# Kernel optimization log

Measured on AMD Instinct MI355X. Metric: run time of the kernel, lower is better.

## Reference

```python
import jax, jax.numpy as jnp
import numpy as np

D = 192          # d_model
H = 8            # n_heads
DH = D // H      # d_head = 24
DFF = 2 * D      # FeedForward hidden = d_model*2
SIZES = [384 + 8 * i for i in range(32)]   # ragged segment lengths
TOTAL = sum(SIZES)                          # 16256
EPS = 1e-5

# static ragged -> padded index maps (numpy, baked at trace time)
_sz = np.asarray(SIZES)
B = len(_sz)
MAXN = int(_sz.max())
SEG = np.repeat(np.arange(B), _sz)                      # [TOTAL] segment id
POS = np.concatenate([np.arange(s) for s in _sz])       # [TOTAL] position in segment
PADMASK = np.ones((B, MAXN), dtype=bool)                # True = padding (key_padding_mask)
PADMASK[SEG, POS] = False


def _layernorm(x, gamma, beta):
    mu = jnp.mean(x, axis=-1, keepdims=True)
    var = jnp.var(x, axis=-1, keepdims=True)
    return (x - mu) * jax.lax.rsqrt(var + EPS) * gamma + beta


def setup_inputs() -> dict:
    key = jax.random.key(0)
    ks = jax.random.split(key, 8)
    w = lambda k, shape: jax.random.normal(k, shape, jnp.float32) * 0.02
    return {
        "x": jax.random.normal(ks[0], (TOTAL, D), jnp.float32),
        "sizes": jnp.asarray(SIZES, jnp.int32),
        "Wqkv": w(ks[1], (3 * D, D)), "bqkv": jnp.zeros((3 * D,), jnp.float32),
        "Wo": w(ks[2], (D, D)),       "bo": jnp.zeros((D,), jnp.float32),
        "Wg": w(ks[3], (D, 2 * D)),   "bg": jnp.zeros((D,), jnp.float32),
        "gamma1": jnp.ones((D,), jnp.float32), "beta1": jnp.zeros((D,), jnp.float32),
        "W1": w(ks[4], (DFF, D)),     "b1": jnp.zeros((DFF,), jnp.float32),
        "W2": w(ks[5], (D, DFF)),     "b2": jnp.zeros((D,), jnp.float32),
        "gamma2": jnp.ones((D,), jnp.float32), "beta2": jnp.zeros((D,), jnp.float32),
    }


def reference(x, sizes, Wqkv, bqkv, Wo, bo, Wg, bg, gamma1, beta1,
              W1, b1, W2, b2, gamma2, beta2):
    # --- pad_by_sizes (vectorized scatter, static index maps) ---
    pad = jnp.zeros((B, MAXN, D), x.dtype).at[SEG, POS].set(x)   # [B, MAXN, D]

    # --- nn.MultiheadAttention (batch_first, key_padding_mask) ---
    qkv = pad @ Wqkv.T + bqkv                                    # [B, MAXN, 3D]
    q, k, v = jnp.split(qkv, 3, axis=-1)
    def heads(t):  # [B, MAXN, D] -> [B, H, MAXN, DH]
        return t.reshape(B, MAXN, H, DH).transpose(0, 2, 1, 3)
    q, k, v = heads(q), heads(k), heads(v)
    scores = jnp.einsum("bhqd,bhkd->bhqk", q, k) / np.sqrt(DH)   # [B, H, MAXN, MAXN]
    scores = jnp.where(PADMASK[:, None, None, :], jnp.float32(-1e9), scores)
    attn = jax.nn.softmax(scores, axis=-1)
    o = jnp.einsum("bhqk,bhkd->bhqd", attn, v)                   # [B, H, MAXN, DH]
    o = o.transpose(0, 2, 1, 3).reshape(B, MAXN, D)
    out = o @ Wo.T + bo                                          # [B, MAXN, D]

    # --- gather back to ragged; gate/norm/ff are per-token, so the torch
    # per-segment loop is equivalent to one vectorized pass over all tokens ---
    out_flat = out[SEG, POS]                                     # [TOTAL, D]
    g = jax.nn.sigmoid(jnp.concatenate([out_flat, x], axis=-1) @ Wg.T + bg)
    h = g * out_flat + (1.0 - g) * x                             # GatedResidual
    h = _layernorm(h, gamma1, beta1)                             # self.norm
    y = jax.nn.silu(h @ W1.T + b1) @ W2.T + b2                   # FeedForward.net
    return _layernorm(h + y, gamma2, beta2)                      # residual + norm
```

## Files before the change

kernel.cpp:

```cpp
#include <hip/hip_runtime.h>
#include <hip/hip_bf16.h>
#include <math.h>

#define D_      192
#define H_      8
#define DH_     24
#define NSEG    32
#define TOTAL_  16256
static constexpr float LN_EPS = 1e-5f;
static constexpr float SCALE  = 0.20412414523193154f;
static constexpr float SC_L2E = 0.29446679331797463f;

typedef float  f32x4  __attribute__((ext_vector_type(4)));
typedef short  bf16x8 __attribute__((ext_vector_type(8)));
typedef unsigned short u16x4 __attribute__((ext_vector_type(4)));
typedef unsigned int   u32x4 __attribute__((ext_vector_type(4)));

__device__ __forceinline__ unsigned short f2b(float f) {
    __hip_bfloat16 h = __float2bfloat16(f);
    return *(unsigned short*)&h;
}
__device__ __forceinline__ unsigned pack2(float a, float b) {
    __hip_bfloat162 h = __float22bfloat162_rn(make_float2(a, b));
    return *(unsigned*)&h;
}
__device__ __forceinline__ float b2f(unsigned short h) {
    union { unsigned u; float f; } v; v.u = (unsigned)h << 16; return v.f;
}
__device__ __forceinline__ float fexp2(float x) {
#if __has_builtin(__builtin_amdgcn_exp2f)
    return __builtin_amdgcn_exp2f(x);
#else
    return exp2f(x);
#endif
}

#define NXE 3121152
__global__ __launch_bounds__(256)
void conv_all(const float* __restrict__ x,
              const float* __restrict__ w0, const float* __restrict__ w1,
              const float* __restrict__ w2, const float* __restrict__ w3,
              const float* __restrict__ w4,
              unsigned short* __restrict__ xb, unsigned short* __restrict__ wb)
{
    int i = (blockIdx.x * 256 + threadIdx.x) * 4;
    const float* src; unsigned short* dst; int off;
    if (i < NXE) { src = x; dst = xb; off = 0; }
    else {
        int j = i - NXE; dst = wb;
        if      (j < 110592) { src = w0; off = 0; }
        else if (j < 147456) { src = w1; off = 110592; }
        else if (j < 221184) { src = w2; off = 147456; }
        else if (j < 294912) { src = w3; off = 221184; }
        else                 { src = w4; off = 294912; }
        i = j;
    }
    float4 v = *(const float4*)&src[i - off];
    u16x4 o = { f2b(v.x), f2b(v.y), f2b(v.z), f2b(v.w) };
    *(u16x4*)&dst[i] = o;
}

template<int KF, int MR, int OUT_BF16>
__global__ __launch_bounds__(256)
void gemm_lds(const unsigned short* __restrict__ Ain,
              const unsigned short* __restrict__ Wb,
              const float* __restrict__ bias,
              void* __restrict__ Cout, int N)
{
    constexpr int KSW = KF * 32 + 8;
    __shared__ unsigned short Wp[64 * KSW];

    const int tid = threadIdx.x;
    const int wv  = tid >> 6;
    const int l   = tid & 63;
    const int m0  = blockIdx.x * (64 * MR) + wv * (16 * MR);
    const int n0  = blockIdx.y * 64;
    const int rl  = l & 15;
    const int kc  = (l >> 4) * 8;

    bf16x8 afrag[MR][KF];
    #pragma unroll
    for (int h = 0; h < MR; ++h)
        #pragma unroll
        for (int kk = 0; kk < KF; ++kk)
            afrag[h][kk] = *(const bf16x8*)&Ain[(size_t)(m0 + h * 16 + rl) * (KF * 32) + kk * 32 + kc];

    #pragma unroll
    for (int i = 0; i < KF; ++i) {
        int u = i * 256 + tid;
        int row = u / (KF * 4), c = u % (KF * 4);
        *(bf16x8*)&Wp[row * KSW + c * 8] = *(const bf16x8*)&Wb[(size_t)(n0 + row) * (KF * 32) + c * 8];
    }
    __syncthreads();

    f32x4 acc[MR][4] = {};
    #pragma unroll
    for (int kk = 0; kk < KF; ++kk) {
        #pragma unroll
        for (int nf = 0; nf < 4; ++nf) {
            bf16x8 b = *(const bf16x8*)&Wp[(nf * 16 + rl) * KSW + kk * 32 + kc];
            #pragma unroll
            for (int h = 0; h < MR; ++h)
                acc[h][nf] = __builtin_amdgcn_mfma_f32_16x16x32_bf16(afrag[h][kk], b, acc[h][nf], 0, 0, 0);
        }
    }

    #pragma unroll
    for (int h = 0; h < MR; ++h) {
        #pragma unroll
        for (int nf = 0; nf < 4; ++nf) {
            const int c = n0 + nf * 16 + rl;
            const float bz = bias[c];
            #pragma unroll
            for (int q = 0; q < 4; ++q) {
                const int r = m0 + h * 16 + (l >> 4) * 4 + q;
                float v = acc[h][nf][q] + bz;
                if (OUT_BF16) ((unsigned short*)Cout)[(size_t)r * N + c] = f2b(v);
                else          ((float*)Cout)[(size_t)r * N + c] = v;
            }
        }
    }
}

__global__ __launch_bounds__(256, 2)
void tail_fused(const unsigned short* __restrict__ o_b,
                const unsigned short* __restrict__ xb,
                const unsigned short* __restrict__ wo_b,
                const unsigned short* __restrict__ wg_b,
                const unsigned short* __restrict__ w1_b,
                const unsigned short* __restrict__ w2_b,
                const float* __restrict__ bo, const float* __restrict__ bg,
                const float* __restrict__ b1, const float* __restrict__ b2,
                const float* __restrict__ gamma1, const float* __restrict__ beta1,
                const float* __restrict__ gamma2, const float* __restrict__ beta2,
                float* __restrict__ out)
{
    constexpr int WS = 200;
    __shared__ unsigned short Wp[96 * WS];
    __shared__ unsigned short Al[64 * WS];

    const int tid = threadIdx.x;
    const int wv  = tid >> 6;
    const int l   = tid & 63;
    const int rl  = l & 15;
    const int g   = l >> 4;
    const int kc  = g * 8;
    const int m0  = blockIdx.x * 64 + wv * 16;

    bf16x8 afA[6];
    #pragma unroll
    for (int kk = 0; kk < 6; ++kk)
        afA[kk] = *(const bf16x8*)&o_b[(size_t)(m0 + rl) * 192 + kk * 32 + kc];

    f32x4 accA[12] = {};
    #pragma unroll
    for (int sub = 0; sub < 2; ++sub) {
        __syncthreads();
        #pragma unroll
        for (int i = 0; i < 9; ++i) {
            int u = i * 256 + tid;
            int row = u / 24, c = u % 24;
            *(bf16x8*)&Wp[row * WS + c * 8] = *(const bf16x8*)&wo_b[(size_t)(sub * 96 + row) * 192 + c * 8];
        }
        __syncthreads();
        #pragma unroll
        for (int kk = 0; kk < 6; ++kk)
            #pragma unroll
            for (int nf2 = 0; nf2 < 6; ++nf2) {
                bf16x8 b = *(const bf16x8*)&Wp[(nf2 * 16 + rl) * WS + kk * 32 + kc];
                accA[sub * 6 + nf2] = __builtin_amdgcn_mfma_f32_16x16x32_bf16(afA[kk], b, accA[sub * 6 + nf2], 0, 0, 0);
            }
    }

    float att[12][4];
    #pragma unroll
    for (int nf = 0; nf < 12; ++nf) {
        const int cnf = (nf / 6) * 96 + (nf % 6) * 16 + rl;
        const float bz = bo[cnf];
        #pragma unroll
        for (int q = 0; q < 4; ++q) {
            att[nf][q] = accA[nf][q] + bz;
            Al[(wv * 16 + g * 4 + q) * WS + cnf] = f2b(att[nf][q]);
        }
    }

    bf16x8 afX[6];
    #pragma unroll
    for (int kk = 0; kk < 6; ++kk)
        afX[kk] = *(const bf16x8*)&xb[(size_t)(m0 + rl) * 192 + kk * 32 + kc];

    f32x4 accB[12] = {};
    #pragma unroll
    for (int kb2 = 0; kb2 < 2; ++kb2)
        #pragma unroll
        for (int sub = 0; sub < 2; ++sub) {
            __syncthreads();
            #pragma unroll
            for (int i = 0; i < 9; ++i) {
                int u = i * 256 + tid;
                int row = u / 24, c = u % 24;
                *(bf16x8*)&Wp[row * WS + c * 8] = *(const bf16x8*)&wg_b[(size_t)(sub * 96 + row) * 384 + kb2 * 192 + c * 8];
            }
            __syncthreads();
            #pragma unroll
            for (int kk = 0; kk < 6; ++kk) {
                bf16x8 a = (kb2 == 0) ? *(const bf16x8*)&Al[(wv * 16 + rl) * WS + kk * 32 + kc]
                                      : afX[kk];
                #pragma unroll
                for (int nf2 = 0; nf2 < 6; ++nf2) {
                    bf16x8 b = *(const bf16x8*)&Wp[(nf2 * 16 + rl) * WS + kk * 32 + kc];
                    accB[sub * 6 + nf2] = __builtin_amdgcn_mfma_f32_16x16x32_bf16(a, b, accB[sub * 6 + nf2], 0, 0, 0);
                }
            }
        }

    float h1ln[12][4];
    {
        float bz[12], gam[12], bet[12];
        #pragma unroll
        for (int nf = 0; nf < 12; ++nf) {
            const int cnf = (nf / 6) * 96 + (nf % 6) * 16 + rl;
            bz[nf]  = bg[cnf];
            gam[nf] = gamma1[cnf];
            bet[nf] = beta1[cnf];
        }
        #pragma unroll
        for (int q = 0; q < 4; ++q) {
            const int r = m0 + g * 4 + q;
            const size_t rb = (size_t)r * 192;
            float h[12];
            float s = 0.f;
            #pragma unroll
            for (int nf = 0; nf < 12; ++nf) {
                const int cnf = (nf / 6) * 96 + (nf % 6) * 16 + rl;
                float v  = accB[nf][q] + bz[nf];
                float gt = 1.f / (1.f + __expf(-v));
                h[nf] = gt * att[nf][q] + (1.f - gt) * b2f(xb[rb + cnf]);
                s += h[nf];
            }
            s += __shfl_xor(s, 1); s += __shfl_xor(s, 2);
            s += __shfl_xor(s, 4); s += __shfl_xor(s, 8);
            const float mu = s * (1.f / 192.f);
            float sq = 0.f;
            #pragma unroll
            for (int nf = 0; nf < 12; ++nf) { float d = h[nf] - mu; sq += d * d; }
            sq += __shfl_xor(sq, 1); sq += __shfl_xor(sq, 2);
            sq += __shfl_xor(sq, 4); sq += __shfl_xor(sq, 8);
            const float rstd = rsqrtf(sq * (1.f / 192.f) + LN_EPS);
            #pragma unroll
            for (int nf = 0; nf < 12; ++nf)
                h1ln[nf][q] = (h[nf] - mu) * rstd * gam[nf] + bet[nf];
        }
    }
    __syncthreads();
    #pragma unroll
    for (int nf = 0; nf < 12; ++nf) {
        const int cnf = (nf / 6) * 96 + (nf % 6) * 16 + rl;
        #pragma unroll
        for (int q = 0; q < 4; ++q)
            Al[(wv * 16 + g * 4 + q) * WS + cnf] = f2b(h1ln[nf][q]);
    }
    __syncthreads();

    bf16x8 afC[6];
    #pragma unroll
    for (int kk = 0; kk < 6; ++kk)
        afC[kk] = *(const bf16x8*)&Al[(wv * 16 + rl) * WS + kk * 32 + kc];

    f32x4 accD[12] = {};
    #pragma unroll
    for (int ch = 0; ch < 2; ++ch) {
        f32x4 accC[12] = {};
        #pragma unroll
        for (int sub = 0; sub < 2; ++sub) {
            __syncthreads();
            #pragma unroll
            for (int i = 0; i < 9; ++i) {
                int u = i * 256 + tid;
                int row = u / 24, c = u % 24;
                *(bf16x8*)&Wp[row * WS + c * 8] = *(const bf16x8*)&w1_b[(size_t)(ch * 192 + sub * 96 + row) * 192 + c * 8];
            }
            __syncthreads();
            #pragma unroll
            for (int kk = 0; kk < 6; ++kk)
                #pragma unroll
                for (int nf2 = 0; nf2 < 6; ++nf2) {
                    bf16x8 b = *(const bf16x8*)&Wp[(nf2 * 16 + rl) * WS + kk * 32 + kc];
                    accC[sub * 6 + nf2] = __builtin_amdgcn_mfma_f32_16x16x32_bf16(afC[kk], b, accC[sub * 6 + nf2], 0, 0, 0);
                }
        }
        __syncthreads();
        #pragma unroll
        for (int nf = 0; nf < 12; ++nf) {
            const int colc = (nf / 6) * 96 + (nf % 6) * 16 + rl;
            const float bz1 = b1[ch * 192 + colc];
            #pragma unroll
            for (int q = 0; q < 4; ++q) {
                float v = accC[nf][q] + bz1;
                float s = 1.f / (1.f + __expf(-v));
                Al[(wv * 16 + g * 4 + q) * WS + colc] = f2b(v * s);
            }
        }
        #pragma unroll
        for (int sub = 0; sub < 2; ++sub) {
            __syncthreads();
            #pragma unroll
            for (int i = 0; i < 9; ++i) {
                int u = i * 256 + tid;
                int row = u / 24, c = u % 24;
                *(bf16x8*)&Wp[row * WS + c * 8] = *(const bf16x8*)&w2_b[(size_t)(sub * 96 + row) * 384 + ch * 192 + c * 8];
            }
            __syncthreads();
            #pragma unroll
            for (int kk = 0; kk < 6; ++kk) {
                bf16x8 a = *(const bf16x8*)&Al[(wv * 16 + rl) * WS + kk * 32 + kc];
                #pragma unroll
                for (int nf2 = 0; nf2 < 6; ++nf2) {
                    bf16x8 b = *(const bf16x8*)&Wp[(nf2 * 16 + rl) * WS + kk * 32 + kc];
                    accD[sub * 6 + nf2] = __builtin_amdgcn_mfma_f32_16x16x32_bf16(a, b, accD[sub * 6 + nf2], 0, 0, 0);
                }
            }
        }
    }

    float bz[12], gam[12], bet[12];
    #pragma unroll
    for (int nf = 0; nf < 12; ++nf) {
        const int cnf = (nf / 6) * 96 + (nf % 6) * 16 + rl;
        bz[nf]  = b2[cnf];
        gam[nf] = gamma2[cnf];
        bet[nf] = beta2[cnf];
    }
    #pragma unroll
    for (int q = 0; q < 4; ++q) {
        const int r = m0 + g * 4 + q;
        const size_t rb = (size_t)r * 192;
        float h[12];
        float s = 0.f;
        #pragma unroll
        for (int nf = 0; nf < 12; ++nf) {
            h[nf] = h1ln[nf][q] + accD[nf][q] + bz[nf];
            s += h[nf];
        }
        s += __shfl_xor(s, 1); s += __shfl_xor(s, 2);
        s += __shfl_xor(s, 4); s += __shfl_xor(s, 8);
        const float mu = s * (1.f / 192.f);
        float sq = 0.f;
        #pragma unroll
        for (int nf = 0; nf < 12; ++nf) { float d = h[nf] - mu; sq += d * d; }
        sq += __shfl_xor(sq, 1); sq += __shfl_xor(sq, 2);
        sq += __shfl_xor(sq, 4); sq += __shfl_xor(sq, 8);
        const float rstd = rsqrtf(sq * (1.f / 192.f) + LN_EPS);
        #pragma unroll
        for (int nf = 0; nf < 12; ++nf) {
            const int cnf = (nf / 6) * 96 + (nf % 6) * 16 + rl;
            out[rb + cnf] = (h[nf] - mu) * rstd * gam[nf] + bet[nf];
        }
    }
}

#define KSTR 40
#define VSTR 72

__global__ __launch_bounds__(256)
void attn_mfma(const unsigned short* __restrict__ qkv, unsigned short* __restrict__ o)
{
    const int w    = blockIdx.x;
    const int xcd  = w & 7;
    const int slot = w >> 3;
    const int seg  = xcd + 8 * (slot / 80);
    const int inr  = slot % 80;
    const int head = inr / 10;
    const int q0   = (inr % 10) * 64;

    const int n    = 384 + 8 * seg;
    const int base = 384 * seg + 4 * seg * (seg - 1);
    if (q0 >= n) return;

    __shared__ unsigned short Ks[2][64 * KSTR];
    __shared__ unsigned short Vt[2][32 * VSTR];

    const int tid = threadIdx.x;
    const int wv  = tid >> 6;
    const int l   = tid & 63;
    const int lq  = l & 15;
    const int g   = l >> 4;

    if (tid < 64) {
        *(uint4*)&Ks[0][tid * KSTR + 24] = make_uint4(0, 0, 0, 0);
        *(uint4*)&Ks[1][tid * KSTR + 24] = make_uint4(0, 0, 0, 0);
    }
    for (int t4 = tid; t4 < 144; t4 += 256) {
        *(unsigned long long*)&Vt[0][24 * VSTR + t4 * 4] = 0ull;
        *(unsigned long long*)&Vt[1][24 * VSTR + t4 * 4] = 0ull;
    }

    const int qrow = q0 + wv * 16 + lq;
    const int qtok = base + (qrow < n ? qrow : n - 1);
    bf16x8 qfrag = {};
    if (g < 3) qfrag = *(const bf16x8*)&qkv[(size_t)qtok * 576 + head * 24 + g * 8];

    const int sj  = tid & 63;
    const int sc  = tid >> 6;
    const int scj = 32 * (sj >> 5) + 8 * ((sj >> 2) & 3) + 4 * ((sj >> 4) & 1) + (sj & 3);

    bf16x8 kreg = {}, vreg = {};
    if (tid < 192) {
        int jr = sj; if (jr >= n) jr = n - 1;
        const unsigned short* rp = &qkv[(size_t)(base + jr) * 576 + head * 24 + sc * 8];
        kreg = *(const bf16x8*)(rp + 192);
        vreg = *(const bf16x8*)(rp + 384);
        *(bf16x8*)&Ks[0][sj * KSTR + sc * 8] = kreg;
        #pragma unroll
        for (int e = 0; e < 8; ++e)
            Vt[0][(sc * 8 + e) * VSTR + scj] = ((const unsigned short*)&vreg)[e];
    }

    float lsum = 0.f;
    f32x4 oacc[2] = {};

    const int nt = (n + 63) >> 6;
    int cur = 0;
    for (int t = 0; t < nt; ++t) {
        __syncthreads();
        const int j0 = t * 64;
        const bool pf = (t + 1 < nt) && (tid < 192);
        if (pf) {
            int jr = j0 + 64 + sj; if (jr >= n) jr = n - 1;
            const unsigned short* rp = &qkv[(size_t)(base + jr) * 576 + head * 24 + sc * 8];
            kreg = *(const bf16x8*)(rp + 192);
            vreg = *(const bf16x8*)(rp + 384);
        }

        bf16x8 kf[4];
        #pragma unroll
        for (int ks = 0; ks < 4; ++ks)
            kf[ks] = *(const bf16x8*)&Ks[cur][(ks * 16 + lq) * KSTR + g * 8];

        const int rem = n - j0;
        f32x4 sacc[4] = {};
        #pragma unroll
        for (int ks = 0; ks < 4; ++ks)
            sacc[ks] = __builtin_amdgcn_mfma_f32_16x16x32_bf16(kf[ks], qfrag, sacc[ks], 0, 0, 0);

        float psum = 0.f;
        unsigned pw[8];
        #pragma unroll
        for (int ks = 0; ks < 4; ++ks) {
            float pv[4];
            #pragma unroll
            for (int r = 0; r < 4; ++r) {
                float p = fexp2(sacc[ks][r] * SC_L2E);
                if (rem < 64) { int key = ks * 16 + g * 4 + r; if (key >= rem) p = 0.f; }
                psum += p;
                pv[r] = p;
            }
            pw[ks * 2 + 0] = pack2(pv[0], pv[1]);
            pw[ks * 2 + 1] = pack2(pv[2], pv[3]);
        }
        psum += __shfl_xor(psum, 16);
        psum += __shfl_xor(psum, 32);
        lsum += psum;

        bf16x8 pfr[2];
        #pragma unroll
        for (int jk = 0; jk < 2; ++jk) {
            u32x4 fr = { pw[jk*4+0], pw[jk*4+1], pw[jk*4+2], pw[jk*4+3] };
            pfr[jk] = *(bf16x8*)&fr;
        }

        #pragma unroll
        for (int jk = 0; jk < 2; ++jk) {
            #pragma unroll
            for (int df = 0; df < 2; ++df) {
                bf16x8 vf = *(const bf16x8*)&Vt[cur][(df * 16 + lq) * VSTR + jk * 32 + g * 8];
                oacc[df] = __builtin_amdgcn_mfma_f32_16x16x32_bf16(vf, pfr[jk], oacc[df], 0, 0, 0);
            }
        }

        if (pf) {
            *(bf16x8*)&Ks[cur ^ 1][sj * KSTR + sc * 8] = kreg;
            #pragma unroll
            for (int e = 0; e < 8; ++e)
                Vt[cur ^ 1][(sc * 8 + e) * VSTR + scj] = ((const unsigned short*)&vreg)[e];
        }
        cur ^= 1;
    }

    if (qrow < n) {
        const float rl2 = 1.f / lsum;
        #pragma unroll
        for (int df = 0; df < 2; ++df) {
            const int d0 = df * 16 + g * 4;
            if (d0 < 24) {
                unsigned w0 = pack2(oacc[df][0] * rl2, oacc[df][1] * rl2);
                unsigned w1 = pack2(oacc[df][2] * rl2, oacc[df][3] * rl2);
                unsigned long long wd = (unsigned long long)w0 | ((unsigned long long)w1 << 32);
                *(unsigned long long*)&o[(size_t)(base + qrow) * 192 + head * 24 + d0] = wd;
            }
        }
    }
}

extern "C" void kernel_launch(void* const* d_in, const int* in_sizes, int n_in,
                              void* d_out, int out_size, void* d_ws, size_t ws_size,
                              hipStream_t stream)
{
    const float* x      = (const float*)d_in[0];
    const float* Wqkv   = (const float*)d_in[2];
    const float* bqkv   = (const float*)d_in[3];
    const float* Wo     = (const float*)d_in[4];
    const float* bo     = (const float*)d_in[5];
    const float* Wg     = (const float*)d_in[6];
    const float* bg     = (const float*)d_in[7];
    const float* gamma1 = (const float*)d_in[8];
    const float* beta1  = (const float*)d_in[9];
    const float* W1     = (const float*)d_in[10];
    const float* b1     = (const float*)d_in[11];
    const float* W2     = (const float*)d_in[12];
    const float* b2     = (const float*)d_in[13];
    const float* gamma2 = (const float*)d_in[14];
    const float* beta2  = (const float*)d_in[15];
    float* out = (float*)d_out;
    float* ws  = (float*)d_ws;

    const size_t T = TOTAL_;
    unsigned short* qkv_b = (unsigned short*)ws;
    unsigned short* o_b   = (unsigned short*)(ws + 288 * T);
    unsigned short* wb    = (unsigned short*)(ws + 384 * T);
    unsigned short* xb    = (unsigned short*)(ws + 396 * T);

    dim3 blk(256);

    conv_all<<<dim3(3408), blk, 0, stream>>>(x, Wqkv, Wo, Wg, W1, W2, xb, wb);
    gemm_lds<6,2,1><<<dim3(127, 9), blk, 0, stream>>>(xb, wb, bqkv, qkv_b, 576);
    attn_mfma<<<dim3(2560), blk, 0, stream>>>(qkv_b, o_b);
    tail_fused<<<dim3(254), blk, 0, stream>>>(o_b, xb, wb + 110592, wb + 147456,
                                              wb + 221184, wb + 294912,
                                              bo, bg, b1, b2,
                                              gamma1, beta1, gamma2, beta2, out);
}
```

Before: 91.94 us.

## Prefetch next weight tile into registers in tail kernel; fold softmax scale into QKV GEMM

The fused tail kernel is restructured into a flat sequence of weight-tile stages in which the next 96-row weight slab is loaded from global memory into registers while the current slab is consumed by MFMA sweeps. This hides global-load latency behind compute instead of serializing load, sync and compute, at the cost of nine extra bf16x8 registers per thread. Separately, the QKV GEMM now multiplies Q columns by scale*log2(e) in its epilogue, which removes a multiply per score in the attention inner loop. That change rounds the scaled Q to bf16, a small precision difference.

```diff
diff --git a/kernel.cpp b/kernel.cpp
--- a/kernel.cpp
+++ b/kernel.cpp
@@ -60,7 +60,7 @@
     *(u16x4*)&dst[i] = o;
 }
 
-template<int KF, int MR, int OUT_BF16>
+template<int KF, int MR, int OUT_BF16, int QS>
 __global__ __launch_bounds__(256)
 void gemm_lds(const unsigned short* __restrict__ Ain,
               const unsigned short* __restrict__ Wb,
@@ -115,12 +115,26 @@
             for (int q = 0; q < 4; ++q) {
                 const int r = m0 + h * 16 + (l >> 4) * 4 + q;
                 float v = acc[h][nf][q] + bz;
+                if (QS && c < 192) v *= SC_L2E;
                 if (OUT_BF16) ((unsigned short*)Cout)[(size_t)r * N + c] = f2b(v);
                 else          ((float*)Cout)[(size_t)r * N + c] = v;
             }
         }
     }
 }
+
+#define LOAD9(BASE, STRIDE) { \
+    _Pragma("unroll") for (int i_ = 0; i_ < 9; ++i_) \
+        wreg[i_] = *(const bf16x8*)&(BASE)[(size_t)rowA[i_] * (STRIDE) + colA[i_] * 8]; }
+#define STAGE9() { \
+    _Pragma("unroll") for (int i_ = 0; i_ < 9; ++i_) \
+        *(bf16x8*)&Wp[rowA[i_] * WS + colA[i_] * 8] = wreg[i_]; }
+#define SWEEP6(ACC, OFF, AEXPR) { \
+    _Pragma("unroll") for (int kk = 0; kk < 6; ++kk) { \
+        bf16x8 a_ = (AEXPR); \
+        _Pragma("unroll") for (int nf2 = 0; nf2 < 6; ++nf2) { \
+            bf16x8 b_ = *(const bf16x8*)&Wp[(nf2 * 16 + rl) * WS + kk * 32 + kc]; \
+            ACC[(OFF) + nf2] = __builtin_amdgcn_mfma_f32_16x16x32_bf16(a_, b_, ACC[(OFF) + nf2], 0, 0, 0); } } }
 
 __global__ __launch_bounds__(256, 2)
 void tail_fused(const unsigned short* __restrict__ o_b,
@@ -147,30 +161,25 @@
     const int kc  = g * 8;
     const int m0  = blockIdx.x * 64 + wv * 16;
 
-    bf16x8 afA[6];
-    #pragma unroll
-    for (int kk = 0; kk < 6; ++kk)
+    int rowA[9], colA[9];
+    #pragma unroll
+    for (int i = 0; i < 9; ++i) { int u = i * 256 + tid; rowA[i] = u / 24; colA[i] = u % 24; }
+    bf16x8 wreg[9];
+
+    bf16x8 afA[6], afX[6];
+    #pragma unroll
+    for (int kk = 0; kk < 6; ++kk) {
         afA[kk] = *(const bf16x8*)&o_b[(size_t)(m0 + rl) * 192 + kk * 32 + kc];
+        afX[kk] = *(const bf16x8*)&xb [(size_t)(m0 + rl) * 192 + kk * 32 + kc];
+    }
+
+    LOAD9(wo_b, 192);
 
     f32x4 accA[12] = {};
-    #pragma unroll
-    for (int sub = 0; sub < 2; ++sub) {
-        __syncthreads();
-        #pragma unroll
-        for (int i = 0; i < 9; ++i) {
-            int u = i * 256 + tid;
-            int row = u / 24, c = u % 24;
-            *(bf16x8*)&Wp[row * WS + c * 8] = *(const bf16x8*)&wo_b[(size_t)(sub * 96 + row) * 192 + c * 8];
-        }
-        __syncthreads();
-        #pragma unroll
-        for (int kk = 0; kk < 6; ++kk)
-            #pragma unroll
-            for (int nf2 = 0; nf2 < 6; ++nf2) {
-                bf16x8 b = *(const bf16x8*)&Wp[(nf2 * 16 + rl) * WS + kk * 32 + kc];
-                accA[sub * 6 + nf2] = __builtin_amdgcn_mfma_f32_16x16x32_bf16(afA[kk], b, accA[sub * 6 + nf2], 0, 0, 0);
-            }
-    }
+    STAGE9(); LOAD9(wo_b + 96 * 192, 192); __syncthreads();
+    SWEEP6(accA, 0, afA[kk]);
+    __syncthreads(); STAGE9(); LOAD9(wg_b, 384); __syncthreads();
+    SWEEP6(accA, 6, afA[kk]);
 
     float att[12][4];
     #pragma unroll
@@ -184,35 +193,15 @@
         }
     }
 
-    bf16x8 afX[6];
-    #pragma unroll
-    for (int kk = 0; kk < 6; ++kk)
-        afX[kk] = *(const bf16x8*)&xb[(size_t)(m0 + rl) * 192 + kk * 32 + kc];
-
     f32x4 accB[12] = {};
-    #pragma unroll
-    for (int kb2 = 0; kb2 < 2; ++kb2)
-        #pragma unroll
-        for (int sub = 0; sub < 2; ++sub) {
-            __syncthreads();
-            #pragma unroll
-            for (int i = 0; i < 9; ++i) {
-                int u = i * 256 + tid;
-                int row = u / 24, c = u % 24;
-                *(bf16x8*)&Wp[row * WS + c * 8] = *(const bf16x8*)&wg_b[(size_t)(sub * 96 + row) * 384 + kb2 * 192 + c * 8];
-            }
-            __syncthreads();
-            #pragma unroll
-            for (int kk = 0; kk < 6; ++kk) {
-                bf16x8 a = (kb2 == 0) ? *(const bf16x8*)&Al[(wv * 16 + rl) * WS + kk * 32 + kc]
-                                      : afX[kk];
-                #pragma unroll
-                for (int nf2 = 0; nf2 < 6; ++nf2) {
-                    bf16x8 b = *(const bf16x8*)&Wp[(nf2 * 16 + rl) * WS + kk * 32 + kc];
-                    accB[sub * 6 + nf2] = __builtin_amdgcn_mfma_f32_16x16x32_bf16(a, b, accB[sub * 6 + nf2], 0, 0, 0);
-                }
-            }
-        }
+    __syncthreads(); STAGE9(); LOAD9(wg_b + 96 * 384, 384); __syncthreads();
+    SWEEP6(accB, 0, (*(const bf16x8*)&Al[(wv * 16 + rl) * WS + kk * 32 + kc]));
+    __syncthreads(); STAGE9(); LOAD9(wg_b + 192, 384); __syncthreads();
+    SWEEP6(accB, 6, (*(const bf16x8*)&Al[(wv * 16 + rl) * WS + kk * 32 + kc]));
+    __syncthreads(); STAGE9(); LOAD9(wg_b + 96 * 384 + 192, 384); __syncthreads();
+    SWEEP6(accB, 0, afX[kk]);
+    __syncthreads(); STAGE9(); LOAD9(w1_b, 192); __syncthreads();
+    SWEEP6(accB, 6, afX[kk]);
 
     float h1ln[12][4];
     {
@@ -252,7 +241,6 @@
                 h1ln[nf][q] = (h[nf] - mu) * rstd * gam[nf] + bet[nf];
         }
     }
-    __syncthreads();
     #pragma unroll
     for (int nf = 0; nf < 12; ++nf) {
         const int cnf = (nf / 6) * 96 + (nf % 6) * 16 + rl;
@@ -260,40 +248,22 @@
         for (int q = 0; q < 4; ++q)
             Al[(wv * 16 + g * 4 + q) * WS + cnf] = f2b(h1ln[nf][q]);
     }
-    __syncthreads();
-
     bf16x8 afC[6];
     #pragma unroll
     for (int kk = 0; kk < 6; ++kk)
         afC[kk] = *(const bf16x8*)&Al[(wv * 16 + rl) * WS + kk * 32 + kc];
 
     f32x4 accD[12] = {};
-    #pragma unroll
-    for (int ch = 0; ch < 2; ++ch) {
+    {
         f32x4 accC[12] = {};
-        #pragma unroll
-        for (int sub = 0; sub < 2; ++sub) {
-            __syncthreads();
-            #pragma unroll
-            for (int i = 0; i < 9; ++i) {
-                int u = i * 256 + tid;
-                int row = u / 24, c = u % 24;
-                *(bf16x8*)&Wp[row * WS + c * 8] = *(const bf16x8*)&w1_b[(size_t)(ch * 192 + sub * 96 + row) * 192 + c * 8];
-            }
-            __syncthreads();
-            #pragma unroll
-            for (int kk = 0; kk < 6; ++kk)
-                #pragma unroll
-                for (int nf2 = 0; nf2 < 6; ++nf2) {
-                    bf16x8 b = *(const bf16x8*)&Wp[(nf2 * 16 + rl) * WS + kk * 32 + kc];
-                    accC[sub * 6 + nf2] = __builtin_amdgcn_mfma_f32_16x16x32_bf16(afC[kk], b, accC[sub * 6 + nf2], 0, 0, 0);
-                }
-        }
-        __syncthreads();
+        __syncthreads(); STAGE9(); LOAD9(w1_b + 96 * 192, 192); __syncthreads();
+        SWEEP6(accC, 0, afC[kk]);
+        __syncthreads(); STAGE9(); LOAD9(w2_b, 384); __syncthreads();
+        SWEEP6(accC, 6, afC[kk]);
         #pragma unroll
         for (int nf = 0; nf < 12; ++nf) {
             const int colc = (nf / 6) * 96 + (nf % 6) * 16 + rl;
-            const float bz1 = b1[ch * 192 + colc];
+            const float bz1 = b1[colc];
             #pragma unroll
             for (int q = 0; q < 4; ++q) {
                 float v = accC[nf][q] + bz1;
@@ -301,26 +271,32 @@
                 Al[(wv * 16 + g * 4 + q) * WS + colc] = f2b(v * s);
             }
         }
-        #pragma unroll
-        for (int sub = 0; sub < 2; ++sub) {
-            __syncthreads();
-            #pragma unroll
-            for (int i = 0; i < 9; ++i) {
-                int u = i * 256 + tid;
-                int row = u / 24, c = u % 24;
-                *(bf16x8*)&Wp[row * WS + c * 8] = *(const bf16x8*)&w2_b[(size_t)(sub * 96 + row) * 384 + ch * 192 + c * 8];
-            }
-            __syncthreads();
-            #pragma unroll
-            for (int kk = 0; kk < 6; ++kk) {
-                bf16x8 a = *(const bf16x8*)&Al[(wv * 16 + rl) * WS + kk * 32 + kc];
-                #pragma unroll
-                for (int nf2 = 0; nf2 < 6; ++nf2) {
-                    bf16x8 b = *(const bf16x8*)&Wp[(nf2 * 16 + rl) * WS + kk * 32 + kc];
-                    accD[sub * 6 + nf2] = __builtin_amdgcn_mfma_f32_16x16x32_bf16(a, b, accD[sub * 6 + nf2], 0, 0, 0);
-                }
-            }
-        }
+        __syncthreads(); STAGE9(); LOAD9(w2_b + 96 * 384, 384); __syncthreads();
+        SWEEP6(accD, 0, (*(const bf16x8*)&Al[(wv * 16 + rl) * WS + kk * 32 + kc]));
+        __syncthreads(); STAGE9(); LOAD9(w1_b + 192 * 192, 192); __syncthreads();
+        SWEEP6(accD, 6, (*(const bf16x8*)&Al[(wv * 16 + rl) * WS + kk * 32 + kc]));
+    }
+    {
+        f32x4 accC[12] = {};
+        __syncthreads(); STAGE9(); LOAD9(w1_b + (192 + 96) * 192, 192); __syncthreads();
+        SWEEP6(accC, 0, afC[kk]);
+        __syncthreads(); STAGE9(); LOAD9(w2_b + 192, 384); __syncthreads();
+        SWEEP6(accC, 6, afC[kk]);
+        #pragma unroll
+        for (int nf = 0; nf < 12; ++nf) {
+            const int colc = (nf / 6) * 96 + (nf % 6) * 16 + rl;
+            const float bz1 = b1[192 + colc];
+            #pragma unroll
+            for (int q = 0; q < 4; ++q) {
+                float v = accC[nf][q] + bz1;
+                float s = 1.f / (1.f + __expf(-v));
+                Al[(wv * 16 + g * 4 + q) * WS + colc] = f2b(v * s);
+            }
+        }
+        __syncthreads(); STAGE9(); LOAD9(w2_b + 96 * 384 + 192, 384); __syncthreads();
+        SWEEP6(accD, 0, (*(const bf16x8*)&Al[(wv * 16 + rl) * WS + kk * 32 + kc]));
+        __syncthreads(); STAGE9(); __syncthreads();
+        SWEEP6(accD, 6, (*(const bf16x8*)&Al[(wv * 16 + rl) * WS + kk * 32 + kc]));
     }
 
     float bz[12], gam[12], bet[12];
@@ -450,7 +426,7 @@
             float pv[4];
             #pragma unroll
             for (int r = 0; r < 4; ++r) {
-                float p = fexp2(sacc[ks][r] * SC_L2E);
+                float p = fexp2(sacc[ks][r]);
                 if (rem < 64) { int key = ks * 16 + g * 4 + r; if (key >= rem) p = 0.f; }
                 psum += p;
                 pv[r] = p;
@@ -533,7 +509,7 @@
     dim3 blk(256);
 
     conv_all<<<dim3(3408), blk, 0, stream>>>(x, Wqkv, Wo, Wg, W1, W2, xb, wb);
-    gemm_lds<6,2,1><<<dim3(127, 9), blk, 0, stream>>>(xb, wb, bqkv, qkv_b, 576);
+    gemm_lds<6,2,1,1><<<dim3(127, 9), blk, 0, stream>>>(xb, wb, bqkv, qkv_b, 576);
     attn_mfma<<<dim3(2560), blk, 0, stream>>>(qkv_b, o_b);
     tail_fused<<<dim3(254), blk, 0, stream>>>(o_b, xb, wb + 110592, wb + 147456,
                                               wb + 221184, wb + 294912,
```

Result: slower. 121.9 us (+32.6%).
